# Optimization experiments

Hardware: AMD Instinct MI355X
Metric: run time of the kernel (lower is better)

Reference implementation:

```python
import jax, jax.numpy as jnp
import numpy as np

C = 256
NH = 8
STRIDE = 4
HD = C // NH
SCALE = HD ** -0.5


def conv2d(x, w, b, stride=1, padding='VALID', groups=1):
    y = jax.lax.conv_general_dilated(
        x, w, (stride, stride), padding,
        dimension_numbers=('NCHW', 'OIHW', 'NCHW'),
        feature_group_count=groups)
    return y + b[None, :, None, None]


def setup_inputs() -> dict:
    key = jax.random.key(0)
    ks = jax.random.split(key, 20)
    s = 0.02
    d = {
        'x': jax.random.normal(ks[0], (8, C, 64, 64), jnp.float32),
        'wq': jax.random.normal(ks[1], (2 * C, C, 1, 1), jnp.float32) * s,
        'bq': jnp.zeros((2 * C,), jnp.float32),
        'ws': jax.random.normal(ks[2], (C, C, STRIDE, STRIDE), jnp.float32) * s,
        'bs': jnp.zeros((C,), jnp.float32),
        'wak_d': jax.random.normal(ks[3], (C, 1, 3, 3), jnp.float32) * s,
        'bak_d': jnp.zeros((C,), jnp.float32),
        'wak_p': jax.random.normal(ks[4], (C, C, 1, 1), jnp.float32) * s,
        'bak_p': jnp.zeros((C,), jnp.float32),
        'wav_d': jax.random.normal(ks[5], (C, 1, 3, 3), jnp.float32) * s,
        'bav_d': jnp.zeros((C,), jnp.float32),
        'wav_p': jax.random.normal(ks[6], (C, C, 1, 1), jnp.float32) * s,
        'bav_p': jnp.zeros((C,), jnp.float32),
        'wek': jax.random.normal(ks[7], (C, C, 1, 1), jnp.float32) * s,
        'bek': jnp.zeros((C,), jnp.float32),
        'wev': jax.random.normal(ks[8], (C, C, 1, 1), jnp.float32) * s,
        'bev': jnp.zeros((C,), jnp.float32),
        'wproj': jax.random.normal(ks[9], (C, 2 * C, 1, 1), jnp.float32) * s,
        'bproj': jnp.zeros((C,), jnp.float32),
    }
    return d


def _heads_kv(t):
    # [B,C,h,w] -> [B,NH,N_kv,HD]
    B = t.shape[0]
    return t.reshape(B, NH, HD, -1).transpose(0, 1, 3, 2)


def _attn_branch(q, k, v):
    # q: [B,NH,Nq,HD], k/v: [B,NH,Nkv,HD]
    attn = jnp.einsum('bhqd,bhkd->bhqk', q, k) * SCALE
    attn = jax.nn.softmax(attn, axis=-1)
    return jnp.einsum('bhqk,bhkd->bhqd', attn, v)


def reference(x, wq, bq, ws, bs, wak_d, bak_d, wak_p, bak_p,
              wav_d, bav_d, wav_p, bav_p, wek, bek, wev, bev, wproj, bproj):
    B, Cc, H, W = x.shape
    # QKV-style 1x1 query projection -> two query sets
    q = conv2d(x, wq, bq)  # [B,2C,H,W]
    q = q.reshape(B, 2, NH, HD, H * W).transpose(1, 0, 2, 4, 3)  # [2,B,NH,HW,HD]
    qa, qe = q[0], q[1]
    # spatial reduction
    xr = conv2d(x, ws, bs, stride=STRIDE)  # [B,C,H/s,W/s]
    spak = _heads_kv(conv2d(conv2d(xr, wak_d, bak_d, padding=[(1, 1), (1, 1)], groups=C), wak_p, bak_p))
    spav = _heads_kv(conv2d(conv2d(xr, wav_d, bav_d, padding=[(1, 1), (1, 1)], groups=C), wav_p, bav_p))
    spek = _heads_kv(conv2d(xr, wek, bek))
    spev = _heads_kv(conv2d(xr, wev, bev))
    outa = _attn_branch(qa, spak, spav).transpose(0, 1, 3, 2).reshape(B, Cc, H, W)
    oute = _attn_branch(qe, spek, spev).transpose(0, 1, 3, 2).reshape(B, Cc, H, W)
    out = jnp.concatenate((outa, oute), axis=1)
    return conv2d(out, wproj, bproj)
```

## Files before the change

### kernel.cpp

```cpp
#include <hip/hip_runtime.h>
#include <hip/hip_bf16.h>

#define QSC (0.17677669529663687f * 1.4426950408889634f)

typedef __attribute__((ext_vector_type(8))) short bf16x8;
typedef __attribute__((ext_vector_type(4))) float f32x4;
typedef unsigned short u16;

union FragU { unsigned u[4]; uint4 q; bf16x8 v; };

__device__ inline u16 f2bu(float a) {
  union { __hip_bfloat16 h; u16 s; } c;
  c.h = __float2bfloat16(a);
  return c.s;
}
__device__ inline unsigned pk2(float lo, float hi) {
  unsigned r;
  asm("v_cvt_pk_bf16_f32 %0, %1, %2" : "=v"(r) : "v"(lo), "v"(hi));
  return r;
}
__device__ inline float exp2r(float x) {
  float r;
  asm("v_exp_f32 %0, %1" : "=v"(r) : "v"(x));
  return r;
}
__device__ inline void gl16(const u16* g, u16* l) {
  __builtin_amdgcn_global_load_lds(
      (const __attribute__((address_space(1))) unsigned int*)g,
      (__attribute__((address_space(3))) unsigned int*)l, 16, 0, 0);
}
__device__ inline void waitvm0() {
  asm volatile("s_waitcnt vmcnt(0)" ::: "memory");
}

__global__ __launch_bounds__(256) void k_xT(
    const float* __restrict__ X, u16* __restrict__ XT,
    const float* __restrict__ wq, const float* __restrict__ wproj,
    const float* __restrict__ ws,
    const float* __restrict__ w0, const float* __restrict__ w1,
    const float* __restrict__ w2, const float* __restrict__ w3,
    u16* __restrict__ wqb, u16* __restrict__ wpb,
    u16* __restrict__ wsb, u16* __restrict__ wkvb) {
  if (blockIdx.z == 8) {
    int which = blockIdx.y;
    int tid = blockIdx.x * 256 + threadIdx.x;
    const int ST = 16384;
    if (which == 0) {
      for (int i = tid; i < 131072; i += ST) wqb[i] = f2bu(wq[i]);
    } else if (which == 1) {
      for (int i = tid; i < 131072; i += ST) wpb[i] = f2bu(wproj[i]);
    } else if (which == 2) {
      for (int i = tid; i < 1048576; i += ST) {
        int co = i >> 12, rem = i & 4095, tap = rem >> 8, ci = rem & 255;
        wsb[i] = f2bu(ws[co * 4096 + ci * 16 + tap]);
      }
    } else if (which < 7) {
      const float* src = (which == 3) ? w0 : (which == 4) ? w1 : (which == 5) ? w2 : w3;
      u16* dst = wkvb + (size_t)(which - 3) * 65536;
      for (int i = tid; i < 65536; i += ST) dst[i] = f2bu(src[i]);
    }
    return;
  }
  __shared__ float L[32 * 65];
  int n0 = blockIdx.x * 64, c0 = blockIdx.y * 32, b = blockIdx.z;
  int t = threadIdx.x;
#pragma unroll
  for (int i = 0; i < 8; ++i) {
    int idx = i * 256 + t;
    int r = idx >> 6, nn = idx & 63;
    L[r * 65 + nn] = X[((size_t)(b * 256 + c0 + r)) * 4096 + n0 + nn];
  }
  __syncthreads();
  int nn = t >> 2, cq = t & 3;
  uint4 u;
  u.x = pk2(L[(cq * 8 + 0) * 65 + nn], L[(cq * 8 + 1) * 65 + nn]);
  u.y = pk2(L[(cq * 8 + 2) * 65 + nn], L[(cq * 8 + 3) * 65 + nn]);
  u.z = pk2(L[(cq * 8 + 4) * 65 + nn], L[(cq * 8 + 5) * 65 + nn]);
  u.w = pk2(L[(cq * 8 + 6) * 65 + nn], L[(cq * 8 + 7) * 65 + nn]);
  *(uint4*)(XT + ((size_t)b * 4096 + n0 + nn) * 256 + c0 + cq * 8) = u;
}

__global__ __launch_bounds__(256) void k_gemm_x(
    const u16* __restrict__ XT, const u16* __restrict__ Wqb,
    const float* __restrict__ bias, u16* __restrict__ Qb,
    const u16* __restrict__ Wsb, float* __restrict__ Psr) {
  __shared__ __align__(16) u16 SM[16384];
  int b = blockIdx.z;
  int t = threadIdx.x, w = t >> 6, l = t & 63, g = l >> 4, lq = l & 15;
  int wr = w >> 1, wc = w & 1;
  const u16* Xb = XT + (size_t)b * 4096 * 256;
  int srow = w * 32 + (l >> 2), scol = (l & 3) * 8;
  u16* lA = SM + w * 1024;
  u16* lB = SM + 8192 + w * 1024;

  f32x4 acc[4][4];
#pragma unroll
  for (int ms = 0; ms < 4; ++ms)
#pragma unroll
    for (int ns = 0; ns < 4; ++ns) acc[ms][ns] = {0.f, 0.f, 0.f, 0.f};

  if (blockIdx.x < 32) {
    int n0 = blockIdx.x * 128, m0 = blockIdx.y * 128;
    const u16* gA = Wqb + (size_t)(m0 + srow) * 256 + scol;
    const u16* gB = Xb + (size_t)(n0 + srow) * 256 + scol;

    gl16(gA, lA); gl16(gA + 16 * 256, lA + 512);
    gl16(gB, lB); gl16(gB + 16 * 256, lB + 512);
    waitvm0();
    __syncthreads();
#pragma unroll
    for (int kt = 0; kt < 8; ++kt) {
      int cur = kt & 1;
      if (kt < 7) {
        int sel = cur ^ 1, ko = (kt + 1) * 32;
        gl16(gA + ko, lA + sel * 4096); gl16(gA + 16 * 256 + ko, lA + sel * 4096 + 512);
        gl16(gB + ko, lB + sel * 4096); gl16(gB + 16 * 256 + ko, lB + sel * 4096 + 512);
      }
      const u16* Ab = SM + cur * 4096;
      const u16* Bb = SM + 8192 + cur * 4096;
      FragU a[4], bb[4];
#pragma unroll
      for (int ms = 0; ms < 4; ++ms)
        a[ms].q = *(const uint4*)(Ab + (wr * 64 + ms * 16 + lq) * 32 + g * 8);
#pragma unroll
      for (int ns = 0; ns < 4; ++ns)
        bb[ns].q = *(const uint4*)(Bb + (wc * 64 + ns * 16 + lq) * 32 + g * 8);
#pragma unroll
      for (int ms = 0; ms < 4; ++ms)
#pragma unroll
        for (int ns = 0; ns < 4; ++ns)
          acc[ms][ns] = __builtin_amdgcn_mfma_f32_16x16x32_bf16(a[ms].v, bb[ns].v, acc[ms][ns], 0, 0, 0);
      waitvm0();
      __syncthreads();
    }

    float bR[4][4];
#pragma unroll
    for (int ms = 0; ms < 4; ++ms)
#pragma unroll
      for (int r = 0; r < 4; ++r) bR[ms][r] = bias[m0 + wr * 64 + ms * 16 + g * 4 + r];

    char* Lc = (char*)SM;
#pragma unroll
    for (int ms = 0; ms < 4; ++ms)
#pragma unroll
      for (int ns = 0; ns < 4; ++ns) {
        int nl = wc * 64 + ns * 16 + lq;
        int mb2 = (wr * 64 + ms * 16 + g * 4) * 2;
        int off = (nl * 256 + mb2) ^ ((nl & 7) << 4);
        *(uint2*)(Lc + off) = make_uint2(
            pk2((acc[ms][ns][0] + bR[ms][0]) * QSC, (acc[ms][ns][1] + bR[ms][1]) * QSC),
            pk2((acc[ms][ns][2] + bR[ms][2]) * QSC, (acc[ms][ns][3] + bR[ms][3]) * QSC));
      }
    __syncthreads();
    int sh0 = m0 >> 5;
#pragma unroll
    for (int rr = 0; rr < 8; ++rr) {
      int idx = rr * 256 + t;
      int ch = idx & 3, shl = (idx >> 2) & 3, nn = idx >> 4;
      int off = (nn * 256 + shl * 64 + ch * 16) ^ ((nn & 7) << 4);
      uint4 v = *(const uint4*)(Lc + off);
      *(uint4*)(Qb + ((size_t)(b * 16 + sh0 + shl) * 4096 + n0 + nn) * 32 + ch * 8) = v;
    }
  } else {
    int ks = blockIdx.x - 32;
    int m0 = (blockIdx.y >> 1) * 128, n0 = (blockIdx.y & 1) * 128;
    const u16* gA = Wsb + (size_t)(m0 + srow) * 4096 + scol;
    int nA = n0 + srow, nB = nA + 16;
    int iA = nA >> 4, jA = nA & 15, iB = nB >> 4, jB = nB & 15;

#define SR_STAGE(sel, kt) {                                                   \
    int ktg = ks * 16 + (kt);                                                 \
    int tap = ktg >> 3, ci0 = (ktg & 7) * 32;                                 \
    int ky = tap >> 2, kx = tap & 3;                                          \
    gl16(gA + ktg * 32, lA + (sel) * 4096);                                   \
    gl16(gA + (size_t)16 * 4096 + ktg * 32, lA + (sel) * 4096 + 512);         \
    int pixA = (4 * iA + ky) * 64 + 4 * jA + kx;                              \
    int pixB = (4 * iB + ky) * 64 + 4 * jB + kx;                              \
    gl16(Xb + (size_t)pixA * 256 + ci0 + scol, lB + (sel) * 4096);            \
    gl16(Xb + (size_t)pixB * 256 + ci0 + scol, lB + (sel) * 4096 + 512); }

    SR_STAGE(0, 0);
    waitvm0();
    __syncthreads();
#pragma unroll
    for (int kt = 0; kt < 16; ++kt) {
      int cur = kt & 1;
      if (kt < 15) SR_STAGE(cur ^ 1, kt + 1);
      const u16* Ab = SM + cur * 4096;
      const u16* Bb = SM + 8192 + cur * 4096;
      FragU a[4], bb[4];
#pragma unroll
      for (int ms = 0; ms < 4; ++ms)
        a[ms].q = *(const uint4*)(Ab + (wr * 64 + ms * 16 + lq) * 32 + g * 8);
#pragma unroll
      for (int ns = 0; ns < 4; ++ns)
        bb[ns].q = *(const uint4*)(Bb + (wc * 64 + ns * 16 + lq) * 32 + g * 8);
#pragma unroll
      for (int ms = 0; ms < 4; ++ms)
#pragma unroll
        for (int ns = 0; ns < 4; ++ns)
          acc[ms][ns] = __builtin_amdgcn_mfma_f32_16x16x32_bf16(a[ms].v, bb[ns].v, acc[ms][ns], 0, 0, 0);
      waitvm0();
      __syncthreads();
    }
#undef SR_STAGE
#pragma unroll
    for (int ms = 0; ms < 4; ++ms)
#pragma unroll
      for (int ns = 0; ns < 4; ++ns) {
        int n = n0 + wc * 64 + ns * 16 + lq;
#pragma unroll
        for (int r = 0; r < 4; ++r) {
          int m = m0 + wr * 64 + ms * 16 + g * 4 + r;
          Psr[(((size_t)ks * 8 + b) * 256 + m) * 256 + n] = acc[ms][ns][r];
        }
      }
  }
}

__global__ __launch_bounds__(256) void k_srdw(
    const float* __restrict__ Psr, const float* __restrict__ bias,
    const float* __restrict__ wkd, const float* __restrict__ bkd,
    const float* __restrict__ wvd, const float* __restrict__ bvd,
    u16* __restrict__ xrT, u16* __restrict__ TKt, u16* __restrict__ TVt) {
  __shared__ float L[16 * 256];
  int cg = blockIdx.x, b = blockIdx.y, t = threadIdx.x;
#pragma unroll
  for (int r = 0; r < 16; ++r) {
    int c = cg * 16 + r;
    float s = bias[c];
#pragma unroll
    for (int ks = 0; ks < 8; ++ks)
      s += Psr[(((size_t)ks * 8 + b) * 256 + c) * 256 + t];
    L[r * 256 + t] = s;
  }
  __syncthreads();
  {
    unsigned wv[8];
#pragma unroll
    for (int r2 = 0; r2 < 8; ++r2)
      wv[r2] = pk2(L[(2 * r2) * 256 + t], L[(2 * r2 + 1) * 256 + t]);
    u16* dst = xrT + ((size_t)b * 256 + t) * 256 + cg * 16;
    *(uint4*)(dst + 0) = make_uint4(wv[0], wv[1], wv[2], wv[3]);
    *(uint4*)(dst + 8) = make_uint4(wv[4], wv[5], wv[6], wv[7]);
  }
  int i = t >> 4, j = t & 15;
  unsigned wk[8], wvv[8];
#pragma unroll
  for (int r2 = 0; r2 < 8; ++r2) {
    int c0 = cg * 16 + 2 * r2;
    float ak0 = bkd[c0], ak1 = bkd[c0 + 1];
    float av0 = bvd[c0], av1 = bvd[c0 + 1];
#pragma unroll
    for (int ky = 0; ky < 3; ++ky) {
      int ii = i + ky - 1;
      if (ii < 0 || ii > 15) continue;
#pragma unroll
      for (int kx = 0; kx < 3; ++kx) {
        int jj = j + kx - 1;
        if (jj < 0 || jj > 15) continue;
        float v0 = L[(2 * r2) * 256 + ii * 16 + jj];
        float v1 = L[(2 * r2 + 1) * 256 + ii * 16 + jj];
        float wk0 = wkd[c0 * 9 + ky * 3 + kx], wk1 = wkd[(c0 + 1) * 9 + ky * 3 + kx];
        float wv0 = wvd[c0 * 9 + ky * 3 + kx], wv1 = wvd[(c0 + 1) * 9 + ky * 3 + kx];
        ak0 = fmaf(v0, wk0, ak0); ak1 = fmaf(v1, wk1, ak1);
        av0 = fmaf(v0, wv0, av0); av1 = fmaf(v1, wv1, av1);
      }
    }
    wk[r2] = pk2(ak0, ak1);
    wvv[r2] = pk2(av0, av1);
  }
  u16* dk = TKt + ((size_t)b * 256 + t) * 256 + cg * 16;
  u16* dv = TVt + ((size_t)b * 256 + t) * 256 + cg * 16;
  *(uint4*)(dk + 0) = make_uint4(wk[0], wk[1], wk[2], wk[3]);
  *(uint4*)(dk + 8) = make_uint4(wk[4], wk[5], wk[6], wk[7]);
  *(uint4*)(dv + 0) = make_uint4(wvv[0], wvv[1], wvv[2], wvv[3]);
  *(uint4*)(dv + 8) = make_uint4(wvv[4], wvv[5], wvv[6], wvv[7]);
}

__global__ __launch_bounds__(256) void k_gemm_kv(
    const u16* __restrict__ xrT, const u16* __restrict__ tkT, const u16* __restrict__ tvT,
    const u16* __restrict__ wkvb,
    const float* __restrict__ bak_p, const float* __restrict__ bav_p,
    const float* __restrict__ bek, const float* __restrict__ bev,
    u16* __restrict__ KV) {
  int which = blockIdx.x, m0 = blockIdx.y * 64, b = blockIdx.z;
  const u16* XT; const float* bias;
  if (which == 0)      { XT = tkT; bias = bak_p; }
  else if (which == 1) { XT = tvT; bias = bav_p; }
  else if (which == 2) { XT = xrT; bias = bek; }
  else                 { XT = xrT; bias = bev; }
  const u16* Wb = wkvb + (size_t)which * 65536;
  int t = threadIdx.x, w = t >> 6, l = t & 63, g = l >> 4, lq = l & 15;
  const u16* Xb = XT + (size_t)b * 65536;
  char* img = (char*)(KV + (size_t)(which * 64 + b * 8) * 8192);
  f32x4 acc[4][4];
#pragma unroll
  for (int ms = 0; ms < 4; ++ms)
#pragma unroll
    for (int ns = 0; ns < 4; ++ns) acc[ms][ns] = {0.f, 0.f, 0.f, 0.f};

  if (!(which & 1)) {
#pragma unroll
    for (int k0 = 0; k0 < 256; k0 += 32) {
      FragU a[4], bb[4];
#pragma unroll
      for (int ms = 0; ms < 4; ++ms)
        a[ms].q = *(const uint4*)(Wb + (size_t)(m0 + ms * 16 + lq) * 256 + k0 + g * 8);
#pragma unroll
      for (int ns = 0; ns < 4; ++ns)
        bb[ns].q = *(const uint4*)(Xb + (size_t)(w * 64 + ns * 16 + lq) * 256 + k0 + g * 8);
#pragma unroll
      for (int ms = 0; ms < 4; ++ms)
#pragma unroll
        for (int ns = 0; ns < 4; ++ns)
          acc[ms][ns] = __builtin_amdgcn_mfma_f32_16x16x32_bf16(a[ms].v, bb[ns].v, acc[ms][ns], 0, 0, 0);
    }
    float bR[4][4];
#pragma unroll
    for (int ms = 0; ms < 4; ++ms)
#pragma unroll
      for (int r = 0; r < 4; ++r) bR[ms][r] = bias[m0 + ms * 16 + g * 4 + r];
#pragma unroll
    for (int ms = 0; ms < 4; ++ms) {
      int mm = m0 + ms * 16 + g * 4;
      int h = mm >> 5, d0 = mm & 31;
      int cb = (d0 >> 3) * 16, e0 = (d0 & 7) * 2;
#pragma unroll
      for (int ns = 0; ns < 4; ++ns) {
        int n = w * 64 + ns * 16 + lq;
        int off = ((n * 64 + cb) ^ (((n >> 1) & 7) << 4)) + e0;
        *(uint2*)(img + (size_t)h * 16384 + off) =
            make_uint2(pk2(acc[ms][ns][0] + bR[ms][0], acc[ms][ns][1] + bR[ms][1]),
                       pk2(acc[ms][ns][2] + bR[ms][2], acc[ms][ns][3] + bR[ms][3]));
      }
    }
  } else {
#pragma unroll
    for (int k0 = 0; k0 < 256; k0 += 32) {
      FragU a[4], bb[4];
#pragma unroll
      for (int ms = 0; ms < 4; ++ms)
        a[ms].q = *(const uint4*)(Wb + (size_t)(m0 + ms * 16 + lq) * 256 + k0 + g * 8);
#pragma unroll
      for (int ns = 0; ns < 4; ++ns)
        bb[ns].q = *(const uint4*)(Xb + (size_t)(w * 64 + ns * 16 + lq) * 256 + k0 + g * 8);
#pragma unroll
      for (int ms = 0; ms < 4; ++ms)
#pragma unroll
        for (int ns = 0; ns < 4; ++ns)
          acc[ms][ns] = __builtin_amdgcn_mfma_f32_16x16x32_bf16(bb[ns].v, a[ms].v, acc[ms][ns], 0, 0, 0);
    }
    float bR[4];
#pragma unroll
    for (int ms = 0; ms < 4; ++ms) bR[ms] = bias[m0 + ms * 16 + lq];
#pragma unroll
    for (int ms = 0; ms < 4; ++ms) {
      int mm = m0 + ms * 16 + lq;
      int h = mm >> 5, d = mm & 31;
      int rowb = d * 512, swz = ((d >> 1) & 7) << 4;
#pragma unroll
      for (int ns = 0; ns < 4; ++ns) {
        int nn = w * 64 + ns * 16 + g * 4;
        int off = (rowb + nn * 2) ^ swz;
        *(uint2*)(img + (size_t)h * 16384 + off) =
            make_uint2(pk2(acc[ms][ns][0] + bR[ms], acc[ms][ns][1] + bR[ms]),
                       pk2(acc[ms][ns][2] + bR[ms], acc[ms][ns][3] + bR[ms]));
      }
    }
  }
}

__global__ __launch_bounds__(256) void k_attn_mfma(
    const u16* __restrict__ Qb, const u16* __restrict__ KV,
    u16* __restrict__ ObT) {
  int h = blockIdx.y, z = blockIdx.z;
  int set = z >> 3, b = z & 7;
  __shared__ __align__(16) u16 Ks[8192];
  __shared__ __align__(16) u16 Vt[8192];
  int t = threadIdx.x, w = t >> 6, l = t & 63;
  {
    const u16* kg = KV + (size_t)((set * 2 + 0) * 64 + b * 8 + h) * 8192;
    const u16* vg = KV + (size_t)((set * 2 + 1) * 64 + b * 8 + h) * 8192;
#pragma unroll
    for (int i = 0; i < 4; ++i) {
      gl16(kg + w * 2048 + i * 512 + l * 8, Ks + w * 2048 + i * 512);
      gl16(vg + w * 2048 + i * 512 + l * 8, Vt + w * 2048 + i * 512);
    }
    waitvm0();
  }
  __syncthreads();

  int lq = l & 15, g = l >> 4;
  int n0 = (blockIdx.x << 7) + w * 32;

  FragU qfA, qfB;
  const u16* qrow = Qb + ((size_t)(b * 16 + set * 8 + h) * 4096 + n0 + lq) * 32 + g * 8;
  qfA.q = *(const uint4*)(qrow);
  qfB.q = *(const uint4*)(qrow + 16 * 32);

  int aA = lq >> 2, cC = lq & 3;
  int lbK = ((aA << 9) + (cC << 6) + (g << 4)) ^ ((cC >> 1) << 4) ^ ((aA & 1) << 6);
  const char* pe = (const char*)Ks + lbK;
  const char* po = (const char*)Ks + ((lbK ^ 32) + 256);

  unsigned pkuA[32], pkuB[32];
#pragma unroll
  for (int k2 = 0; k2 < 8; ++k2) {
    FragU af;
    f32x4 cA, cB;
    af.q = *(const uint4*)(pe + k2 * 2048);
    __builtin_amdgcn_s_setprio(1);
    cA = {0.f, 0.f, 0.f, 0.f};
    cA = __builtin_amdgcn_mfma_f32_16x16x32_bf16(af.v, qfA.v, cA, 0, 0, 0);
    cB = {0.f, 0.f, 0.f, 0.f};
    cB = __builtin_amdgcn_mfma_f32_16x16x32_bf16(af.v, qfB.v, cB, 0, 0, 0);
    __builtin_amdgcn_s_setprio(0);
    pkuA[4 * k2 + 0] = pk2(exp2r(cA[0]), exp2r(cA[1]));
    pkuA[4 * k2 + 1] = pk2(exp2r(cA[2]), exp2r(cA[3]));
    pkuB[4 * k2 + 0] = pk2(exp2r(cB[0]), exp2r(cB[1]));
    pkuB[4 * k2 + 1] = pk2(exp2r(cB[2]), exp2r(cB[3]));
    af.q = *(const uint4*)(po + k2 * 2048);
    __builtin_amdgcn_s_setprio(1);
    cA = {0.f, 0.f, 0.f, 0.f};
    cA = __builtin_amdgcn_mfma_f32_16x16x32_bf16(af.v, qfA.v, cA, 0, 0, 0);
    cB = {0.f, 0.f, 0.f, 0.f};
    cB = __builtin_amdgcn_mfma_f32_16x16x32_bf16(af.v, qfB.v, cB, 0, 0, 0);
    __builtin_amdgcn_s_setprio(0);
    pkuA[4 * k2 + 2] = pk2(exp2r(cA[0]), exp2r(cA[1]));
    pkuA[4 * k2 + 3] = pk2(exp2r(cA[2]), exp2r(cA[3]));
    pkuB[4 * k2 + 2] = pk2(exp2r(cB[0]), exp2r(cB[1]));
    pkuB[4 * k2 + 3] = pk2(exp2r(cB[2]), exp2r(cB[3]));
  }
  __syncthreads();

  int lbV = (lq << 9) + ((g << 4) ^ ((lq & 6) << 3));
  int kb = (lq >> 3) & 1;
  const char* pp = (const char*)Vt + (lbV + kb * 64);
  const char* pm = (const char*)Vt + (lbV - kb * 64);

  FragU ones;
  ones.u[0] = ones.u[1] = ones.u[2] = ones.u[3] = 0x3F803F80u;
  f32x4 oA0 = {0.f, 0.f, 0.f, 0.f}, oA1 = {0.f, 0.f, 0.f, 0.f};
  f32x4 oB0 = {0.f, 0.f, 0.f, 0.f}, oB1 = {0.f, 0.f, 0.f, 0.f};
  f32x4 saA = {0.f, 0.f, 0.f, 0.f}, saB = {0.f, 0.f, 0.f, 0.f};
  __builtin_amdgcn_s_setprio(1);
#pragma unroll
  for (int kv = 0; kv < 8; ++kv) {
    FragU pbA, pbB;
    pbA.u[0] = pkuA[4 * kv + 0]; pbA.u[1] = pkuA[4 * kv + 1];
    pbA.u[2] = pkuA[4 * kv + 2]; pbA.u[3] = pkuA[4 * kv + 3];
    pbB.u[0] = pkuB[4 * kv + 0]; pbB.u[1] = pkuB[4 * kv + 1];
    pbB.u[2] = pkuB[4 * kv + 2]; pbB.u[3] = pkuB[4 * kv + 3];
    const char* pv = (kv & 1) ? pm : pp;
    FragU va0, va1;
    va0.q = *(const uint4*)(pv + kv * 64);
    va1.q = *(const uint4*)(pv + kv * 64 + 8192);
    oA0 = __builtin_amdgcn_mfma_f32_16x16x32_bf16(va0.v, pbA.v, oA0, 0, 0, 0);
    oA1 = __builtin_amdgcn_mfma_f32_16x16x32_bf16(va1.v, pbA.v, oA1, 0, 0, 0);
    oB0 = __builtin_amdgcn_mfma_f32_16x16x32_bf16(va0.v, pbB.v, oB0, 0, 0, 0);
    oB1 = __builtin_amdgcn_mfma_f32_16x16x32_bf16(va1.v, pbB.v, oB1, 0, 0, 0);
    saA = __builtin_amdgcn_mfma_f32_16x16x32_bf16(ones.v, pbA.v, saA, 0, 0, 0);
    saB = __builtin_amdgcn_mfma_f32_16x16x32_bf16(ones.v, pbB.v, saB, 0, 0, 0);
  }
  __builtin_amdgcn_s_setprio(0);

  float invA = __builtin_amdgcn_rcpf(saA[0]);
  float invB = __builtin_amdgcn_rcpf(saB[0]);
  {
    char* ob = (char*)Ks;
    int nnA = w * 32 + lq, nnB = nnA + 16;
    *(uint2*)(ob + nnA * 80 + g * 8) =
        make_uint2(pk2(oA0[0] * invA, oA0[1] * invA), pk2(oA0[2] * invA, oA0[3] * invA));
    *(uint2*)(ob + nnA * 80 + 32 + g * 8) =
        make_uint2(pk2(oA1[0] * invA, oA1[1] * invA), pk2(oA1[2] * invA, oA1[3] * invA));
    *(uint2*)(ob + nnB * 80 + g * 8) =
        make_uint2(pk2(oB0[0] * invB, oB0[1] * invB), pk2(oB0[2] * invB, oB0[3] * invB));
    *(uint2*)(ob + nnB * 80 + 32 + g * 8) =
        make_uint2(pk2(oB1[0] * invB, oB1[1] * invB), pk2(oB1[2] * invB, oB1[3] * invB));
  }
  __syncthreads();
#pragma unroll
  for (int rep = 0; rep < 2; ++rep) {
    int idx = rep * 256 + t;
    int nn = idx >> 2, dq = idx & 3;
    uint4 v = *(const uint4*)((const char*)Ks + nn * 80 + dq * 16);
    *(uint4*)(ObT + ((size_t)b * 4096 + (blockIdx.x << 7) + nn) * 512 +
              set * 256 + h * 32 + dq * 8) = v;
  }
}

__global__ __launch_bounds__(256) void k_gemm_proj(
    const u16* __restrict__ XT, const u16* __restrict__ Wb,
    const float* __restrict__ bias, float* __restrict__ Y) {
  __shared__ __align__(16) u16 SM[16384];
  int n0 = blockIdx.x * 128, m0 = blockIdx.y * 128, b = blockIdx.z;
  int t = threadIdx.x, w = t >> 6, l = t & 63, g = l >> 4, lq = l & 15;
  int wr = w >> 1, wc = w & 1;
  const u16* Xb = XT + (size_t)b * 4096 * 512;
  int srow = w * 32 + (l >> 2), scol = (l & 3) * 8;
  const u16* gA = Wb + (size_t)(m0 + srow) * 512 + scol;
  const u16* gB = Xb + (size_t)(n0 + srow) * 512 + scol;
  u16* lA = SM + w * 1024;
  u16* lB = SM + 8192 + w * 1024;

  f32x4 acc[4][4];
#pragma unroll
  for (int ms = 0; ms < 4; ++ms)
#pragma unroll
    for (int ns = 0; ns < 4; ++ns) acc[ms][ns] = {0.f, 0.f, 0.f, 0.f};

  gl16(gA, lA); gl16(gA + 16 * 512, lA + 512);
  gl16(gB, lB); gl16(gB + 16 * 512, lB + 512);
  waitvm0();
  __syncthreads();
#pragma unroll
  for (int kt = 0; kt < 16; ++kt) {
    int cur = kt & 1;
    if (kt < 15) {
      int sel = cur ^ 1, ko = (kt + 1) * 32;
      gl16(gA + ko, lA + sel * 4096); gl16(gA + 16 * 512 + ko, lA + sel * 4096 + 512);
      gl16(gB + ko, lB + sel * 4096); gl16(gB + 16 * 512 + ko, lB + sel * 4096 + 512);
    }
    const u16* Ab = SM + cur * 4096;
    const u16* Bb = SM + 8192 + cur * 4096;
    FragU a[4], bb[4];
#pragma unroll
    for (int ms = 0; ms < 4; ++ms)
      a[ms].q = *(const uint4*)(Ab + (wr * 64 + ms * 16 + lq) * 32 + g * 8);
#pragma unroll
    for (int ns = 0; ns < 4; ++ns)
      bb[ns].q = *(const uint4*)(Bb + (wc * 64 + ns * 16 + lq) * 32 + g * 8);
#pragma unroll
    for (int ms = 0; ms < 4; ++ms)
#pragma unroll
      for (int ns = 0; ns < 4; ++ns)
        acc[ms][ns] = __builtin_amdgcn_mfma_f32_16x16x32_bf16(a[ms].v, bb[ns].v, acc[ms][ns], 0, 0, 0);
    waitvm0();
    __syncthreads();
  }
#pragma unroll
  for (int ms = 0; ms < 4; ++ms)
#pragma unroll
    for (int ns = 0; ns < 4; ++ns) {
      int n = n0 + wc * 64 + ns * 16 + lq;
#pragma unroll
      for (int r = 0; r < 4; ++r) {
        int m = m0 + wr * 64 + ms * 16 + g * 4 + r;
        Y[((size_t)b * 256 + m) * 4096 + n] = acc[ms][ns][r] + bias[m];
      }
    }
}


extern "C" void kernel_launch(void* const* d_in, const int* in_sizes, int n_in,
                              void* d_out, int out_size, void* d_ws, size_t ws_size,
                              hipStream_t stream) {
  (void)in_sizes; (void)n_in; (void)out_size; (void)ws_size;
  const float* x     = (const float*)d_in[0];
  const float* wq    = (const float*)d_in[1];
  const float* bq    = (const float*)d_in[2];
  const float* wsw   = (const float*)d_in[3];
  const float* bs    = (const float*)d_in[4];
  const float* wak_d = (const float*)d_in[5];
  const float* bak_d = (const float*)d_in[6];
  const float* wak_p = (const float*)d_in[7];
  const float* bak_p = (const float*)d_in[8];
  const float* wav_d = (const float*)d_in[9];
  const float* bav_d = (const float*)d_in[10];
  const float* wav_p = (const float*)d_in[11];
  const float* bav_p = (const float*)d_in[12];
  const float* wek   = (const float*)d_in[13];
  const float* bek   = (const float*)d_in[14];
  const float* wev   = (const float*)d_in[15];
  const float* bev   = (const float*)d_in[16];
  const float* wproj = (const float*)d_in[17];
  const float* bproj = (const float*)d_in[18];
  float* out = (float*)d_out;

  char* p = (char*)d_ws;
  u16* xbT  = (u16*)p;   p += (size_t)8 * 4096 * 256 * 2;
  u16* qb   = (u16*)p;   p += (size_t)8 * 16 * 4096 * 32 * 2;
  u16* obT  = (u16*)p;   p += (size_t)8 * 4096 * 512 * 2;
  float* psr = (float*)p; p += (size_t)8 * 8 * 256 * 256 * 4;
  u16* xrT  = (u16*)p;   p += (size_t)524288 * 2;
  u16* tkT  = (u16*)p;   p += (size_t)524288 * 2;
  u16* tvT  = (u16*)p;   p += (size_t)524288 * 2;
  u16* kvimg = (u16*)p;  p += (size_t)4 * 64 * 8192 * 2;
  u16* wqb  = (u16*)p;   p += (size_t)131072 * 2;
  u16* wpb  = (u16*)p;   p += (size_t)131072 * 2;
  u16* wsb  = (u16*)p;   p += (size_t)1048576 * 2;
  u16* wkvb = (u16*)p;   p += (size_t)262144 * 2;

  k_xT<<<dim3(64, 8, 9), 256, 0, stream>>>(x, xbT, wq, wproj, wsw,
                                           wak_p, wav_p, wek, wev,
                                           wqb, wpb, wsb, wkvb);
  k_gemm_x<<<dim3(40, 4, 8), 256, 0, stream>>>(xbT, wqb, bq, qb, wsb, psr);
  k_srdw<<<dim3(16, 8), 256, 0, stream>>>(psr, bs, wak_d, bak_d, wav_d, bav_d,
                                          xrT, tkT, tvT);
  k_gemm_kv<<<dim3(4, 4, 8), 256, 0, stream>>>(xrT, tkT, tvT, wkvb,
                                               bak_p, bav_p, bek, bev, kvimg);
  k_attn_mfma<<<dim3(32, 8, 16), 256, 0, stream>>>(qb, kvimg, obT);
  k_gemm_proj<<<dim3(32, 2, 8), 256, 0, stream>>>(obT, wpb, bproj, out);
}
```

Baseline: 122.5 us.

## Remove split-K from strided conv GEMM and fuse bias/transpose into epilogue

The spatial-reduction conv GEMM no longer splits K across 8 blocks. Each output tile block now loops over the full K and writes the biased fp32 result plus a transposed bf16 copy directly. This removes the large fp32 partial-sum buffer and the reduction in the depthwise kernel. In exchange, 32 blocks each run a 128-step serial K loop, which can lengthen the critical path of the combined kernel.

```diff
diff --git a/kernel.cpp b/kernel.cpp
--- a/kernel.cpp
+++ b/kernel.cpp
@@ -83,7 +83,8 @@
 __global__ __launch_bounds__(256) void k_gemm_x(
     const u16* __restrict__ XT, const u16* __restrict__ Wqb,
     const float* __restrict__ bias, u16* __restrict__ Qb,
-    const u16* __restrict__ Wsb, float* __restrict__ Psr) {
+    const u16* __restrict__ Wsb, const float* __restrict__ bs,
+    float* __restrict__ xr, u16* __restrict__ xrT) {
   __shared__ __align__(16) u16 SM[16384];
   int b = blockIdx.z;
   int t = threadIdx.x, w = t >> 6, l = t & 63, g = l >> 4, lq = l & 15;
@@ -99,8 +100,8 @@
 #pragma unroll
     for (int ns = 0; ns < 4; ++ns) acc[ms][ns] = {0.f, 0.f, 0.f, 0.f};
 
-  if (blockIdx.x < 32) {
-    int n0 = blockIdx.x * 128, m0 = blockIdx.y * 128;
+  if (blockIdx.x > 0) {
+    int n0 = (blockIdx.x - 1) * 128, m0 = blockIdx.y * 128;
     const u16* gA = Wqb + (size_t)(m0 + srow) * 256 + scol;
     const u16* gB = Xb + (size_t)(n0 + srow) * 256 + scol;
 
@@ -163,88 +164,84 @@
       *(uint4*)(Qb + ((size_t)(b * 16 + sh0 + shl) * 4096 + n0 + nn) * 32 + ch * 8) = v;
     }
   } else {
-    int ks = blockIdx.x - 32;
     int m0 = (blockIdx.y >> 1) * 128, n0 = (blockIdx.y & 1) * 128;
     const u16* gA = Wsb + (size_t)(m0 + srow) * 4096 + scol;
     int nA = n0 + srow, nB = nA + 16;
     int iA = nA >> 4, jA = nA & 15, iB = nB >> 4, jB = nB & 15;
 
-#define SR_STAGE(sel, kt) {                                                   \
-    int ktg = ks * 16 + (kt);                                                 \
-    int tap = ktg >> 3, ci0 = (ktg & 7) * 32;                                 \
+#define SR_STAGE(sel, ktg) {                                                  \
+    int tap = (ktg) >> 3, ci0 = ((ktg) & 7) * 32;                             \
     int ky = tap >> 2, kx = tap & 3;                                          \
-    gl16(gA + ktg * 32, lA + (sel) * 4096);                                   \
-    gl16(gA + (size_t)16 * 4096 + ktg * 32, lA + (sel) * 4096 + 512);         \
+    gl16(gA + (ktg) * 32, lA + (sel) * 4096);                                 \
+    gl16(gA + (size_t)16 * 4096 + (ktg) * 32, lA + (sel) * 4096 + 512);       \
     int pixA = (4 * iA + ky) * 64 + 4 * jA + kx;                              \
     int pixB = (4 * iB + ky) * 64 + 4 * jB + kx;                              \
     gl16(Xb + (size_t)pixA * 256 + ci0 + scol, lB + (sel) * 4096);            \
     gl16(Xb + (size_t)pixB * 256 + ci0 + scol, lB + (sel) * 4096 + 512); }
 
+#define SR_COMP(cur) {                                                        \
+    const u16* Ab = SM + (cur) * 4096;                                        \
+    const u16* Bb = SM + 8192 + (cur) * 4096;                                 \
+    FragU a[4], bb[4];                                                        \
+    _Pragma("unroll")                                                         \
+    for (int ms = 0; ms < 4; ++ms)                                            \
+      a[ms].q = *(const uint4*)(Ab + (wr * 64 + ms * 16 + lq) * 32 + g * 8);  \
+    _Pragma("unroll")                                                         \
+    for (int ns = 0; ns < 4; ++ns)                                            \
+      bb[ns].q = *(const uint4*)(Bb + (wc * 64 + ns * 16 + lq) * 32 + g * 8); \
+    _Pragma("unroll")                                                         \
+    for (int ms = 0; ms < 4; ++ms)                                            \
+      _Pragma("unroll")                                                       \
+      for (int ns = 0; ns < 4; ++ns)                                          \
+        acc[ms][ns] = __builtin_amdgcn_mfma_f32_16x16x32_bf16(                \
+            a[ms].v, bb[ns].v, acc[ms][ns], 0, 0, 0); }
+
     SR_STAGE(0, 0);
     waitvm0();
     __syncthreads();
-#pragma unroll
-    for (int kt = 0; kt < 16; ++kt) {
-      int cur = kt & 1;
-      if (kt < 15) SR_STAGE(cur ^ 1, kt + 1);
-      const u16* Ab = SM + cur * 4096;
-      const u16* Bb = SM + 8192 + cur * 4096;
-      FragU a[4], bb[4];
-#pragma unroll
-      for (int ms = 0; ms < 4; ++ms)
-        a[ms].q = *(const uint4*)(Ab + (wr * 64 + ms * 16 + lq) * 32 + g * 8);
-#pragma unroll
-      for (int ns = 0; ns < 4; ++ns)
-        bb[ns].q = *(const uint4*)(Bb + (wc * 64 + ns * 16 + lq) * 32 + g * 8);
-#pragma unroll
-      for (int ms = 0; ms < 4; ++ms)
-#pragma unroll
-        for (int ns = 0; ns < 4; ++ns)
-          acc[ms][ns] = __builtin_amdgcn_mfma_f32_16x16x32_bf16(a[ms].v, bb[ns].v, acc[ms][ns], 0, 0, 0);
+    for (int k2 = 0; k2 < 64; ++k2) {
+      SR_STAGE(1, 2 * k2 + 1);
+      SR_COMP(0);
       waitvm0();
       __syncthreads();
+      if (k2 < 63) SR_STAGE(0, 2 * k2 + 2);
+      SR_COMP(1);
+      waitvm0();
+      __syncthreads();
     }
 #undef SR_STAGE
+#undef SR_COMP
 #pragma unroll
     for (int ms = 0; ms < 4; ++ms)
 #pragma unroll
       for (int ns = 0; ns < 4; ++ns) {
         int n = n0 + wc * 64 + ns * 16 + lq;
-#pragma unroll
-        for (int r = 0; r < 4; ++r) {
-          int m = m0 + wr * 64 + ms * 16 + g * 4 + r;
-          Psr[(((size_t)ks * 8 + b) * 256 + m) * 256 + n] = acc[ms][ns][r];
-        }
+        int mb = m0 + wr * 64 + ms * 16 + g * 4;
+        float v0 = acc[ms][ns][0] + bs[mb + 0];
+        float v1 = acc[ms][ns][1] + bs[mb + 1];
+        float v2 = acc[ms][ns][2] + bs[mb + 2];
+        float v3 = acc[ms][ns][3] + bs[mb + 3];
+        xr[((size_t)(b * 256) + mb + 0) * 256 + n] = v0;
+        xr[((size_t)(b * 256) + mb + 1) * 256 + n] = v1;
+        xr[((size_t)(b * 256) + mb + 2) * 256 + n] = v2;
+        xr[((size_t)(b * 256) + mb + 3) * 256 + n] = v3;
+        *(uint2*)(xrT + ((size_t)(b * 256) + n) * 256 + mb) =
+            make_uint2(pk2(v0, v1), pk2(v2, v3));
       }
   }
 }
 
 __global__ __launch_bounds__(256) void k_srdw(
-    const float* __restrict__ Psr, const float* __restrict__ bias,
+    const float* __restrict__ xr,
     const float* __restrict__ wkd, const float* __restrict__ bkd,
     const float* __restrict__ wvd, const float* __restrict__ bvd,
-    u16* __restrict__ xrT, u16* __restrict__ TKt, u16* __restrict__ TVt) {
+    u16* __restrict__ TKt, u16* __restrict__ TVt) {
   __shared__ float L[16 * 256];
   int cg = blockIdx.x, b = blockIdx.y, t = threadIdx.x;
 #pragma unroll
-  for (int r = 0; r < 16; ++r) {
-    int c = cg * 16 + r;
-    float s = bias[c];
-#pragma unroll
-    for (int ks = 0; ks < 8; ++ks)
-      s += Psr[(((size_t)ks * 8 + b) * 256 + c) * 256 + t];
-    L[r * 256 + t] = s;
-  }
+  for (int r = 0; r < 16; ++r)
+    L[r * 256 + t] = xr[((size_t)(b * 256 + cg * 16 + r)) * 256 + t];
   __syncthreads();
-  {
-    unsigned wv[8];
-#pragma unroll
-    for (int r2 = 0; r2 < 8; ++r2)
-      wv[r2] = pk2(L[(2 * r2) * 256 + t], L[(2 * r2 + 1) * 256 + t]);
-    u16* dst = xrT + ((size_t)b * 256 + t) * 256 + cg * 16;
-    *(uint4*)(dst + 0) = make_uint4(wv[0], wv[1], wv[2], wv[3]);
-    *(uint4*)(dst + 8) = make_uint4(wv[4], wv[5], wv[6], wv[7]);
-  }
   int i = t >> 4, j = t & 15;
   unsigned wk[8], wvv[8];
 #pragma unroll
@@ -583,7 +580,7 @@
   u16* xbT  = (u16*)p;   p += (size_t)8 * 4096 * 256 * 2;
   u16* qb   = (u16*)p;   p += (size_t)8 * 16 * 4096 * 32 * 2;
   u16* obT  = (u16*)p;   p += (size_t)8 * 4096 * 512 * 2;
-  float* psr = (float*)p; p += (size_t)8 * 8 * 256 * 256 * 4;
+  float* xr  = (float*)p; p += (size_t)524288 * 4;
   u16* xrT  = (u16*)p;   p += (size_t)524288 * 2;
   u16* tkT  = (u16*)p;   p += (size_t)524288 * 2;
   u16* tvT  = (u16*)p;   p += (size_t)524288 * 2;
@@ -596,9 +593,10 @@
   k_xT<<<dim3(64, 8, 9), 256, 0, stream>>>(x, xbT, wq, wproj, wsw,
                                            wak_p, wav_p, wek, wev,
                                            wqb, wpb, wsb, wkvb);
-  k_gemm_x<<<dim3(40, 4, 8), 256, 0, stream>>>(xbT, wqb, bq, qb, wsb, psr);
-  k_srdw<<<dim3(16, 8), 256, 0, stream>>>(psr, bs, wak_d, bak_d, wav_d, bav_d,
-                                          xrT, tkT, tvT);
+  k_gemm_x<<<dim3(33, 4, 8), 256, 0, stream>>>(xbT, wqb, bq, qb, wsb, bs,
+                                               xr, xrT);
+  k_srdw<<<dim3(16, 8), 256, 0, stream>>>(xr, wak_d, bak_d, wav_d, bav_d,
+                                          tkT, tvT);
   k_gemm_kv<<<dim3(4, 4, 8), 256, 0, stream>>>(xrT, tkT, tvT, wkvb,
                                                bak_p, bav_p, bek, bev, kvimg);
   k_attn_mfma<<<dim3(32, 8, 16), 256, 0, stream>>>(qb, kvimg, obT);
```

After: 185.0 us. +51.1%, slower.
